# Performance work log

Hardware: AMD Instinct MI355X
Metric: run time of the kernel (lower is better)

## Reference

```python
import jax, jax.numpy as jnp
from jax import lax
import numpy as np

N = 32768; K = 8; M = 8192; G = 32; EF = 128

def _lrelu(x):
    return jnp.where(x > 0, x, 0.01 * x)

def _pc_res(x, W1, b1, W2, b2):
    h = _lrelu(x @ W1 + b1) @ W2 + b2
    return _lrelu(h + x)

def _conv3d(x, w, b):
    dn = ('NCDHW', 'OIDHW', 'NCDHW')
    return lax.conv_general_dilated(x, w, (1, 1, 1), 'SAME', dimension_numbers=dn) + b[None, :, None, None, None]

def setup_inputs():
    key = jax.random.key(0)
    ks = jax.random.split(key, 32)
    f32 = jnp.float32
    pc_KNN_idx = jax.random.randint(ks[0], (N * K,), 0, N, dtype=jnp.int32)
    pc_KNN_xyz = jax.random.normal(ks[1], (N * K, 3), dtype=f32)
    flat = jax.random.permutation(ks[2], G * G * G)[:M]  # unique voxel coords -> deterministic scatter
    voxel_xyz_int = jnp.stack([flat // (G * G), (flat // G) % G, flat % G], axis=1).astype(jnp.int32)
    voxel_KNN_idx = jax.random.randint(ks[3], (M * K,), 0, N, dtype=jnp.int32)
    voxel_KNN_xyz = jax.random.normal(ks[4], (M * K, 3), dtype=f32)
    s = 0.05
    def rn(i, shape):
        return jax.random.normal(ks[i], shape, dtype=f32) * s
    return dict(
        pc_KNN_idx=pc_KNN_idx, pc_KNN_xyz=pc_KNN_xyz, voxel_xyz_int=voxel_xyz_int,
        voxel_KNN_idx=voxel_KNN_idx, voxel_KNN_xyz=voxel_KNN_xyz,
        pcf_W1=rn(5, (3, EF)), pcf_b1=rn(6, (EF,)), pcf_W2=rn(7, (EF, EF)), pcf_b2=rn(8, (EF,)),
        pcres_W1=rn(9, (7, EF, EF)), pcres_b1=rn(10, (7, EF)),
        pcres_W2=rn(11, (7, EF, EF)), pcres_b2=rn(12, (7, EF)),
        pcc_W1=rn(13, (6, EF + 3, EF)), pcc_b1=rn(14, (6, EF)),
        pcc_W2=rn(15, (6, EF, EF)), pcc_b2=rn(16, (6, EF)),
        r3_Wc1=rn(17, (8, EF, EF, 3, 3, 3)), r3_bc1=rn(18, (8, EF)),
        r3_Wc2=rn(19, (8, EF, EF, 1, 1, 1)), r3_bc2=rn(20, (8, EF)),
        lin1_W=rn(21, (EF, EF)), lin1_b=rn(22, (EF,)),
        lin2_W=rn(23, (EF, EF)), lin2_b=rn(24, (EF,)),
        linb_W=rn(25, (EF, 3)), linb_b=rn(26, (3,)),
    )

def reference(pc_KNN_idx, pc_KNN_xyz, voxel_xyz_int, voxel_KNN_idx, voxel_KNN_xyz,
              pcf_W1, pcf_b1, pcf_W2, pcf_b2,
              pcres_W1, pcres_b1, pcres_W2, pcres_b2,
              pcc_W1, pcc_b1, pcc_W2, pcc_b2,
              r3_Wc1, r3_bc1, r3_Wc2, r3_bc2,
              lin1_W, lin1_b, lin2_W, lin2_b, linb_W, linb_b):
    # pc_conv_first: MLP on KNN relative xyz, max-pool over K neighbors -> [N, EF]
    out = _lrelu(pc_KNN_xyz @ pcf_W1 + pcf_b1) @ pcf_W2 + pcf_b2
    out = jnp.max(out.reshape(-1, K, EF), axis=1)
    out = _lrelu(out)
    out = _pc_res(out, pcres_W1[0], pcres_b1[0], pcres_W2[0], pcres_b2[0])
    for i in range(6):
        idx = pc_KNN_idx if i < 5 else voxel_KNN_idx
        xyz = pc_KNN_xyz if i < 5 else voxel_KNN_xyz
        g = jnp.concatenate([out[idx], xyz], axis=1)            # [R*K, EF+3]
        h = _lrelu(g @ pcc_W1[i] + pcc_b1[i]) @ pcc_W2[i] + pcc_b2[i]
        out = _lrelu(jnp.max(h.reshape(-1, K, EF), axis=1))     # [R, EF]
        out = _pc_res(out, pcres_W1[i + 1], pcres_b1[i + 1], pcres_W2[i + 1], pcres_b2[i + 1])
    # scatter voxel features into a dense grid (coords are unique)
    vi = voxel_xyz_int - jnp.min(voxel_xyz_int, axis=0)
    grid = jnp.zeros((G, G, G, EF), jnp.float32).at[vi[:, 0], vi[:, 1], vi[:, 2]].set(out)
    x = grid.transpose(3, 0, 1, 2)[None]                        # [1, EF, G, G, G]
    for i in range(8):
        y = _lrelu(_conv3d(x, r3_Wc1[i], r3_bc1[i]))
        y = _conv3d(y, r3_Wc2[i], r3_bc2[i])
        x = _lrelu(y + x)
    out = x[0].transpose(1, 2, 3, 0)[vi[:, 0], vi[:, 1], vi[:, 2]]  # gather back [M, EF]
    out = _lrelu(out @ lin1_W + lin1_b)
    out = _lrelu(out @ lin2_W + lin2_b)
    return jax.nn.sigmoid(out @ linb_W + linb_b)                # out_bool head [M, 3]
```

## Files before the change

### kernel.cpp

```cpp
#include <hip/hip_runtime.h>
#include <math.h>

#define EF 128
#define NPTS 32768
#define KNN 8
#define MVOX 8192
#define GDIM 32
#define NVOXG (GDIM*GDIM*GDIM)

typedef __attribute__((ext_vector_type(8))) short bfrag;
typedef __attribute__((ext_vector_type(4))) float f32x4;

__device__ __forceinline__ float lrelu(float x) { return x > 0.f ? x : 0.01f * x; }
__device__ __forceinline__ short f2b(float f) {
    unsigned u = __float_as_uint(f);
    return (short)((u + 0x7fff + ((u >> 16) & 1)) >> 16);
}
#define MFMA(a,b,c) __builtin_amdgcn_mfma_f32_16x16x32_bf16((a),(b),(c),0,0,0)
__device__ __forceinline__ int swz(int row, int bytecol) {
    return row * 256 + (bytecol ^ ((row & 7) << 4));
}

__global__ void k_pack_w(const float* __restrict__ src, short* __restrict__ dst,
                         int K_real, int n_steps, int k_str, int c_str) {
    int t = blockIdx.x * 256 + threadIdx.x;
    int total = n_steps * 4096;
    if (t >= total) return;
    int r = t & 7, l = (t >> 3) & 63, ct = (t >> 9) & 7, s = t >> 12;
    int k = s * 32 + (l >> 4) * 8 + r;
    int col = ct * 16 + (l & 15);
    float v = (k < K_real) ? src[(size_t)k * k_str + (size_t)col * c_str] : 0.f;
    dst[t] = f2b(v);
}
__global__ void k_pack_wc1(const float* __restrict__ src, short* __restrict__ dst) {
    int t = blockIdx.x * 256 + threadIdx.x;
    if (t >= 108 * 4096) return;
    int r = t & 7, l = (t >> 3) & 63, ct = (t >> 9) & 7, s = t >> 12;
    int tap = s >> 2;
    int ci = (s & 3) * 32 + (l >> 4) * 8 + r;
    int col = ct * 16 + (l & 15);
    dst[t] = f2b(src[((size_t)col * 128 + ci) * 27 + tap]);
}


__global__ __launch_bounds__(512) void k_pcfirst(
    const float* __restrict__ xyz, const short* __restrict__ w1p, const float* __restrict__ b1,
    const short* __restrict__ w2p, const float* __restrict__ b2,
    const short* __restrict__ rw1p, const float* __restrict__ rb1,
    const short* __restrict__ rw2p, const float* __restrict__ rb2,
    float* __restrict__ out32, short* __restrict__ out16) {
    __shared__ __align__(16) char tb[32768];
    int wid = threadIdx.x >> 6, lane = threadIdx.x & 63, lrow = lane & 15, lq = lane >> 4;
    int wm = wid >> 2, wn = wid & 3;
    int rowbase = blockIdx.x * 128;
    f32x4 zv = {0.f, 0.f, 0.f, 0.f};
    {
        f32x4 acc1[4][2];
        #pragma unroll
        for (int rt = 0; rt < 4; ++rt) { acc1[rt][0] = zv; acc1[rt][1] = zv; }
        bfrag Bv[2];
        #pragma unroll
        for (int ct = 0; ct < 2; ++ct) Bv[ct] = ((const bfrag*)w1p)[(wn * 2 + ct) * 64 + lane];
        #pragma unroll
        for (int rt = 0; rt < 4; ++rt) {
            bfrag a4;
            #pragma unroll
            for (int r = 0; r < 8; ++r) a4[r] = 0;
            if (lq == 0) {
                int gr = rowbase + wm * 64 + rt * 16 + lrow;
                a4[0] = f2b(xyz[gr * 3]); a4[1] = f2b(xyz[gr * 3 + 1]); a4[2] = f2b(xyz[gr * 3 + 2]);
            }
            #pragma unroll
            for (int ct = 0; ct < 2; ++ct) acc1[rt][ct] = MFMA(a4, Bv[ct], acc1[rt][ct]);
        }
        float bb1[2];
        #pragma unroll
        for (int ct = 0; ct < 2; ++ct) bb1[ct] = b1[wn * 32 + ct * 16 + lrow];
        #pragma unroll
        for (int rt = 0; rt < 4; ++rt)
            #pragma unroll
            for (int ct = 0; ct < 2; ++ct)
                #pragma unroll
                for (int r = 0; r < 4; ++r) {
                    int row = wm * 64 + rt * 16 + lq * 4 + r, col = wn * 32 + ct * 16 + lrow;
                    *(short*)(tb + swz(row, col * 2)) = f2b(lrelu(acc1[rt][ct][r] + bb1[ct]));
                }
    }
    __syncthreads();
    float bb2[2];
    #pragma unroll
    for (int ct = 0; ct < 2; ++ct) bb2[ct] = b2[wn * 32 + ct * 16 + lrow];
    f32x4 acc[4][2];
    #pragma unroll
    for (int rt = 0; rt < 4; ++rt) { acc[rt][0] = zv; acc[rt][1] = zv; }
    const bfrag* bp2 = (const bfrag*)w2p;
    #pragma unroll
    for (int s = 0; s < 4; ++s) {
        bfrag Bv[2];
        #pragma unroll
        for (int ct = 0; ct < 2; ++ct) Bv[ct] = bp2[(s * 8 + wn * 2 + ct) * 64 + lane];
        bfrag av[4];
        #pragma unroll
        for (int rt = 0; rt < 4; ++rt) {
            int row = wm * 64 + rt * 16 + lrow;
            av[rt] = *(const bfrag*)(tb + swz(row, s * 64 + lq * 16));
        }
        #pragma unroll
        for (int ct = 0; ct < 2; ++ct)
            #pragma unroll
            for (int rt = 0; rt < 4; ++rt) acc[rt][ct] = MFMA(av[rt], Bv[ct], acc[rt][ct]);
    }
    float pv[4][2];
    #pragma unroll
    for (int rt = 0; rt < 4; ++rt)
        #pragma unroll
        for (int ct = 0; ct < 2; ++ct) {
            float m = -INFINITY;
            #pragma unroll
            for (int r = 0; r < 4; ++r) m = fmaxf(m, acc[rt][ct][r] + bb2[ct]);
            m = fmaxf(m, __shfl_xor(m, 16, 64));
            pv[rt][ct] = lrelu(m);
        }
    __syncthreads();
    float* xf = (float*)(tb + 4096);
    char*  tres = tb + 12544;
    if ((lq & 1) == 0) {
        #pragma unroll
        for (int rt = 0; rt < 4; ++rt)
            #pragma unroll
            for (int ct = 0; ct < 2; ++ct) {
                int row = wm * 8 + rt * 2 + (lq >> 1), col = wn * 32 + ct * 16 + lrow;
                *(short*)(tb + swz(row, col * 2)) = f2b(pv[rt][ct]);
                xf[row * 130 + col] = pv[rt][ct];
            }
    }
    __syncthreads();
    {
        f32x4 r1 = zv;
        #pragma unroll
        for (int s = 0; s < 4; ++s) {
            bfrag B = ((const bfrag*)rw1p)[(s * 8 + wid) * 64 + lane];
            bfrag a = *(const bfrag*)(tb + swz(lrow, s * 64 + lq * 16));
            r1 = MFMA(a, B, r1);
        }
        float rb1v = rb1[wid * 16 + lrow];
        #pragma unroll
        for (int r = 0; r < 4; ++r) {
            int row = lq * 4 + r;
            *(short*)(tres + swz(row, (wid * 16 + lrow) * 2)) = f2b(lrelu(r1[r] + rb1v));
        }
    }
    __syncthreads();
    {
        f32x4 r2 = zv;
        #pragma unroll
        for (int s = 0; s < 4; ++s) {
            bfrag B = ((const bfrag*)rw2p)[(s * 8 + wid) * 64 + lane];
            bfrag a = *(const bfrag*)(tres + swz(lrow, s * 64 + lq * 16));
            r2 = MFMA(a, B, r2);
        }
        float rb2v = rb2[wid * 16 + lrow];
        int p0 = blockIdx.x * 16;
        #pragma unroll
        for (int r = 0; r < 4; ++r) {
            int row = lq * 4 + r, col = wid * 16 + lrow;
            float v = lrelu(r2[r] + rb2v + xf[row * 130 + col]);
            size_t o = (size_t)(p0 + row) * 128 + col;
            out16[o] = f2b(v);
            if (out32) out32[o] = v;
        }
    }
}

__global__ __launch_bounds__(512) void k_pcconv(
    const short* __restrict__ fin16, const int* __restrict__ idx, const float* __restrict__ xyz,
    const short* __restrict__ w1p, const float* __restrict__ b1,
    const short* __restrict__ w2p, const float* __restrict__ b2,
    const short* __restrict__ rw1p, const float* __restrict__ rb1,
    const short* __restrict__ rw2p, const float* __restrict__ rb2,
    float* __restrict__ out32, short* __restrict__ out16) {
    __shared__ __align__(16) char tb[32768];
    int wid = threadIdx.x >> 6, lane = threadIdx.x & 63, lrow = lane & 15, lq = lane >> 4;
    int wm = wid >> 2, wn = wid & 3;
    int rowbase = blockIdx.x * 128;
    f32x4 zv = {0.f, 0.f, 0.f, 0.f};
    {
        int srow = threadIdx.x >> 2, sseg = threadIdx.x & 3;
        int nb = idx[rowbase + srow];
        const bfrag* src = (const bfrag*)(fin16 + (size_t)nb * 128);
        #pragma unroll
        for (int j = 0; j < 4; ++j) {
            int seg = sseg + j * 4;
            bfrag v = src[seg];
            *(bfrag*)(tb + swz(srow, seg * 16)) = v;
        }
    }
    __syncthreads();
    float bb1[2], bb2[2];
    #pragma unroll
    for (int ct = 0; ct < 2; ++ct) {
        bb1[ct] = b1[wn * 32 + ct * 16 + lrow];
        bb2[ct] = b2[wn * 32 + ct * 16 + lrow];
    }
    f32x4 acc[4][2];
    #pragma unroll
    for (int rt = 0; rt < 4; ++rt) { acc[rt][0] = zv; acc[rt][1] = zv; }
    const bfrag* bp1 = (const bfrag*)w1p;
    #pragma unroll
    for (int s = 0; s < 4; ++s) {
        bfrag Bv[2];
        #pragma unroll
        for (int ct = 0; ct < 2; ++ct) Bv[ct] = bp1[(s * 8 + wn * 2 + ct) * 64 + lane];
        bfrag av[4];
        #pragma unroll
        for (int rt = 0; rt < 4; ++rt) {
            int row = wm * 64 + rt * 16 + lrow;
            av[rt] = *(const bfrag*)(tb + swz(row, s * 64 + lq * 16));
        }
        #pragma unroll
        for (int ct = 0; ct < 2; ++ct)
            #pragma unroll
            for (int rt = 0; rt < 4; ++rt) acc[rt][ct] = MFMA(av[rt], Bv[ct], acc[rt][ct]);
    }
    {
        bfrag Bv[2];
        #pragma unroll
        for (int ct = 0; ct < 2; ++ct) Bv[ct] = bp1[(32 + wn * 2 + ct) * 64 + lane];
        #pragma unroll
        for (int rt = 0; rt < 4; ++rt) {
            bfrag a4;
            #pragma unroll
            for (int r = 0; r < 8; ++r) a4[r] = 0;
            if (lq == 0) {
                int gr = rowbase + wm * 64 + rt * 16 + lrow;
                a4[0] = f2b(xyz[gr * 3]); a4[1] = f2b(xyz[gr * 3 + 1]); a4[2] = f2b(xyz[gr * 3 + 2]);
            }
            #pragma unroll
            for (int ct = 0; ct < 2; ++ct) acc[rt][ct] = MFMA(a4, Bv[ct], acc[rt][ct]);
        }
    }
    __syncthreads();
    #pragma unroll
    for (int rt = 0; rt < 4; ++rt)
        #pragma unroll
        for (int ct = 0; ct < 2; ++ct)
            #pragma unroll
            for (int r = 0; r < 4; ++r) {
                int row = wm * 64 + rt * 16 + lq * 4 + r, col = wn * 32 + ct * 16 + lrow;
                *(short*)(tb + swz(row, col * 2)) = f2b(lrelu(acc[rt][ct][r] + bb1[ct]));
            }
    __syncthreads();
    f32x4 acc2[4][2];
    #pragma unroll
    for (int rt = 0; rt < 4; ++rt) { acc2[rt][0] = zv; acc2[rt][1] = zv; }
    const bfrag* bp2 = (const bfrag*)w2p;
    #pragma unroll
    for (int s = 0; s < 4; ++s) {
        bfrag Bv[2];
        #pragma unroll
        for (int ct = 0; ct < 2; ++ct) Bv[ct] = bp2[(s * 8 + wn * 2 + ct) * 64 + lane];
        bfrag av[4];
        #pragma unroll
        for (int rt = 0; rt < 4; ++rt) {
            int row = wm * 64 + rt * 16 + lrow;
            av[rt] = *(const bfrag*)(tb + swz(row, s * 64 + lq * 16));
        }
        #pragma unroll
        for (int ct = 0; ct < 2; ++ct)
            #pragma unroll
            for (int rt = 0; rt < 4; ++rt) acc2[rt][ct] = MFMA(av[rt], Bv[ct], acc2[rt][ct]);
    }
    float pv[4][2];
    #pragma unroll
    for (int rt = 0; rt < 4; ++rt)
        #pragma unroll
        for (int ct = 0; ct < 2; ++ct) {
            float m = -INFINITY;
            #pragma unroll
            for (int r = 0; r < 4; ++r) m = fmaxf(m, acc2[rt][ct][r] + bb2[ct]);
            m = fmaxf(m, __shfl_xor(m, 16, 64));
            pv[rt][ct] = lrelu(m);
        }
    __syncthreads();
    float* xf = (float*)(tb + 4096);
    char*  tres = tb + 12544;
    if ((lq & 1) == 0) {
        #pragma unroll
        for (int rt = 0; rt < 4; ++rt)
            #pragma unroll
            for (int ct = 0; ct < 2; ++ct) {
                int row = wm * 8 + rt * 2 + (lq >> 1), col = wn * 32 + ct * 16 + lrow;
                *(short*)(tb + swz(row, col * 2)) = f2b(pv[rt][ct]);
                xf[row * 130 + col] = pv[rt][ct];
            }
    }
    __syncthreads();
    {
        f32x4 r1 = zv;
        #pragma unroll
        for (int s = 0; s < 4; ++s) {
            bfrag B = ((const bfrag*)rw1p)[(s * 8 + wid) * 64 + lane];
            bfrag a = *(const bfrag*)(tb + swz(lrow, s * 64 + lq * 16));
            r1 = MFMA(a, B, r1);
        }
        float rb1v = rb1[wid * 16 + lrow];
        #pragma unroll
        for (int r = 0; r < 4; ++r) {
            int row = lq * 4 + r;
            *(short*)(tres + swz(row, (wid * 16 + lrow) * 2)) = f2b(lrelu(r1[r] + rb1v));
        }
    }
    __syncthreads();
    {
        f32x4 r2 = zv;
        #pragma unroll
        for (int s = 0; s < 4; ++s) {
            bfrag B = ((const bfrag*)rw2p)[(s * 8 + wid) * 64 + lane];
            bfrag a = *(const bfrag*)(tres + swz(lrow, s * 64 + lq * 16));
            r2 = MFMA(a, B, r2);
        }
        float rb2v = rb2[wid * 16 + lrow];
        int p0 = blockIdx.x * 16;
        #pragma unroll
        for (int r = 0; r < 4; ++r) {
            int row = lq * 4 + r, col = wid * 16 + lrow;
            float v = lrelu(r2[r] + rb2v + xf[row * 130 + col]);
            size_t o = (size_t)(p0 + row) * 128 + col;
            out16[o] = f2b(v);
            if (out32) out32[o] = v;
        }
    }
}

__global__ __launch_bounds__(512) void k_conv3(
    const float* __restrict__ gin32, const short* __restrict__ gin16,
    const short* __restrict__ w1p, const float* __restrict__ b1,
    const short* __restrict__ w2p, const float* __restrict__ b2,
    float* __restrict__ gout32, short* __restrict__ gout16) {
    __shared__ __align__(16) char Ab[65536];
    int wid = threadIdx.x >> 6, lane = threadIdx.x & 63, lrow = lane & 15, lq = lane >> 4;
    int kg = wid & 1, wn = (wid >> 1) & 1, wm = wid >> 2;
    int va = blockIdx.x >> 3, vb0 = (blockIdx.x & 7) * 4;
    bfrag zf;
    #pragma unroll
    for (int r = 0; r < 8; ++r) zf[r] = 0;
    f32x4 zv = {0.f, 0.f, 0.f, 0.f};
    f32x4 acc[4][4];
    #pragma unroll
    for (int rt = 0; rt < 4; ++rt)
        #pragma unroll
        for (int ct = 0; ct < 4; ++ct) acc[rt][ct] = zv;
    const bfrag* bp1 = (const bfrag*)w1p;

    #pragma unroll 1
    for (int dai = 0; dai < 3; ++dai) {
        __syncthreads();
        {
            int aa = va + dai - 1;
            bool aok = (unsigned)aa < 32u;
            #pragma unroll
            for (int j = 0; j < 6; ++j) {
                int task = (int)threadIdx.x + j * 512;
                int srow = task >> 4, seg = task & 15;
                int bl = srow >> 5, c = srow & 31;
                int sb = vb0 - 1 + bl;
                bool ok = aok && ((unsigned)sb < 32u);
                size_t gb = ok ? ((size_t)((aa * 32 + sb) * 32 + c) * 128 + seg * 8) : 0;
                bfrag v = *((const bfrag*)gin16 + gb / 8);
                *(bfrag*)(Ab + swz(srow, seg * 16)) = ok ? v : zf;
            }
        }
        __syncthreads();
        #pragma unroll
        for (int t9 = 0; t9 < 9; ++t9) {
            int db = t9 / 3 - 1, dc = t9 % 3 - 1;
            int tap = dai * 9 + t9;
            #pragma unroll
            for (int ss = 0; ss < 2; ++ss) {
                int s = kg * 2 + ss;
                bfrag Bv[4];
                #pragma unroll
                for (int ct = 0; ct < 4; ++ct)
                    Bv[ct] = bp1[((tap * 4 + s) * 8 + wn * 4 + ct) * 64 + lane];
                bfrag av[4];
                #pragma unroll
                for (int rt = 0; rt < 4; ++rt) {
                    int ci = ((rt & 1) << 4) + lrow + dc;
                    bool ok = (unsigned)ci < 32u;
                    int srow2 = (wm * 2 + db + 1 + (rt >> 1)) * 32 + (ok ? ci : 0);
                    bfrag t = *(const bfrag*)(Ab + swz(srow2, s * 64 + lq * 16));
                    av[rt] = ok ? t : zf;
                }
                #pragma unroll
                for (int ct = 0; ct < 4; ++ct)
                    #pragma unroll
                    for (int rt = 0; rt < 4; ++rt) acc[rt][ct] = MFMA(av[rt], Bv[ct], acc[rt][ct]);
            }
        }
    }
    __syncthreads();
    if (kg == 1) {
        int p = wm * 2 + wn;
        #pragma unroll
        for (int rt = 0; rt < 4; ++rt)
            #pragma unroll
            for (int ct = 0; ct < 4; ++ct)
                *(f32x4*)(Ab + p * 16384 + ((rt * 4 + ct) * 64 + lane) * 16) = acc[rt][ct];
    }
    __syncthreads();
    if (kg == 0) {
        int p = wm * 2 + wn;
        #pragma unroll
        for (int rt = 0; rt < 4; ++rt)
            #pragma unroll
            for (int ct = 0; ct < 4; ++ct)
                acc[rt][ct] += *(const f32x4*)(Ab + p * 16384 + ((rt * 4 + ct) * 64 + lane) * 16);
    }
    __syncthreads();
    if (kg == 0) {
        float bb1[4];
        #pragma unroll
        for (int ct = 0; ct < 4; ++ct) bb1[ct] = b1[wn * 64 + ct * 16 + lrow];
        #pragma unroll
        for (int rt = 0; rt < 4; ++rt)
            #pragma unroll
            for (int ct = 0; ct < 4; ++ct)
                #pragma unroll
                for (int r = 0; r < 4; ++r) {
                    int row = wm * 64 + rt * 16 + lq * 4 + r, col = wn * 64 + ct * 16 + lrow;
                    *(short*)(Ab + swz(row, col * 2)) = f2b(lrelu(acc[rt][ct][r] + bb1[ct]));
                }
    }
    __syncthreads();
    int wm2 = wid >> 2, wn2 = wid & 3;
    float bb2[2];
    #pragma unroll
    for (int ct = 0; ct < 2; ++ct) bb2[ct] = b2[wn2 * 32 + ct * 16 + lrow];
    f32x4 acc2[4][2];
    #pragma unroll
    for (int rt = 0; rt < 4; ++rt) { acc2[rt][0] = zv; acc2[rt][1] = zv; }
    const bfrag* bp2 = (const bfrag*)w2p;
    #pragma unroll
    for (int s = 0; s < 4; ++s) {
        bfrag Bv[2];
        #pragma unroll
        for (int ct = 0; ct < 2; ++ct) Bv[ct] = bp2[(s * 8 + wn2 * 2 + ct) * 64 + lane];
        bfrag av[4];
        #pragma unroll
        for (int rt = 0; rt < 4; ++rt) {
            int row = wm2 * 64 + rt * 16 + lrow;
            av[rt] = *(const bfrag*)(Ab + swz(row, s * 64 + lq * 16));
        }
        #pragma unroll
        for (int ct = 0; ct < 2; ++ct)
            #pragma unroll
            for (int rt = 0; rt < 4; ++rt) acc2[rt][ct] = MFMA(av[rt], Bv[ct], acc2[rt][ct]);
    }
    #pragma unroll
    for (int rt = 0; rt < 4; ++rt)
        #pragma unroll
        for (int ct = 0; ct < 2; ++ct)
            #pragma unroll
            for (int r = 0; r < 4; ++r) {
                int row = wm2 * 64 + rt * 16 + lq * 4 + r;
                int voxel = (va * 32 + vb0 + (row >> 5)) * 32 + (row & 31);
                size_t o = (size_t)voxel * 128 + wn2 * 32 + ct * 16 + lrow;
                float v = lrelu(acc2[rt][ct][r] + bb2[ct] + gin32[o]);
                gout32[o] = v; gout16[o] = f2b(v);
            }
}

__global__ __launch_bounds__(512) void k_head(
    const short* __restrict__ g16, const int* __restrict__ vx, const int* __restrict__ vmin,
    const short* __restrict__ w1p, const float* __restrict__ b1,
    const short* __restrict__ w2p, const float* __restrict__ b2,
    const float* __restrict__ W3, const float* __restrict__ b3,
    float* __restrict__ out) {
    __shared__ __align__(16) char tb[16384];
    __shared__ float t2[64][129];
    int wid = threadIdx.x >> 6, lane = threadIdx.x & 63, lrow = lane & 15, lq = lane >> 4;
    int rowbase = blockIdx.x * 64;
    int goff[4];
    #pragma unroll
    for (int rt = 0; rt < 4; ++rt) {
        int m = rowbase + rt * 16 + lrow;
        int v0 = vx[m * 3 + 0] - vmin[0];
        int v1 = vx[m * 3 + 1] - vmin[1];
        int v2 = vx[m * 3 + 2] - vmin[2];
        goff[rt] = ((v0 * 32 + v1) * 32 + v2) * 128;
    }
    float bb1 = b1[wid * 16 + lrow], bb2 = b2[wid * 16 + lrow];
    f32x4 zv = {0.f, 0.f, 0.f, 0.f};
    f32x4 acc[4];
    #pragma unroll
    for (int rt = 0; rt < 4; ++rt) acc[rt] = zv;
    const bfrag* bp1 = (const bfrag*)w1p;
    #pragma unroll
    for (int s = 0; s < 4; ++s) {
        bfrag B = bp1[(s * 8 + wid) * 64 + lane];
        #pragma unroll
        for (int rt = 0; rt < 4; ++rt) {
            bfrag a = *((const bfrag*)(g16 + goff[rt]) + s * 4 + lq);
            acc[rt] = MFMA(a, B, acc[rt]);
        }
    }
    #pragma unroll
    for (int rt = 0; rt < 4; ++rt)
        #pragma unroll
        for (int r = 0; r < 4; ++r) {
            int row = rt * 16 + lq * 4 + r, col = wid * 16 + lrow;
            *(short*)(tb + swz(row, col * 2)) = f2b(lrelu(acc[rt][r] + bb1));
        }
    __syncthreads();
    f32x4 acc2[4];
    #pragma unroll
    for (int rt = 0; rt < 4; ++rt) acc2[rt] = zv;
    const bfrag* bp2 = (const bfrag*)w2p;
    #pragma unroll
    for (int s = 0; s < 4; ++s) {
        bfrag B = bp2[(s * 8 + wid) * 64 + lane];
        #pragma unroll
        for (int rt = 0; rt < 4; ++rt) {
            int row = rt * 16 + lrow;
            bfrag av = *(const bfrag*)(tb + swz(row, s * 64 + lq * 16));
            acc2[rt] = MFMA(av, B, acc2[rt]);
        }
    }
    #pragma unroll
    for (int rt = 0; rt < 4; ++rt)
        #pragma unroll
        for (int r = 0; r < 4; ++r) {
            int row = rt * 16 + lq * 4 + r, col = wid * 16 + lrow;
            t2[row][col] = lrelu(acc2[rt][r] + bb2);
        }
    __syncthreads();
    if (threadIdx.x < 192) {
        int row = threadIdx.x & 63, c = threadIdx.x >> 6;
        float s = b3[c];
        #pragma unroll 4
        for (int k = 0; k < 128; ++k) s += t2[row][k] * W3[k * 3 + c];
        out[(size_t)(rowbase + row) * 3 + c] = 1.f / (1.f + expf(-s));
    }
}

__global__ void k_vmin(const int* __restrict__ vx, int M, int* __restrict__ vmin) {
    __shared__ int sm[3 * 256];
    int t = threadIdx.x;
    int m0 = 0x7fffffff, m1 = 0x7fffffff, m2 = 0x7fffffff;
    for (int i = t; i < M; i += 256) {
        m0 = min(m0, vx[i * 3 + 0]); m1 = min(m1, vx[i * 3 + 1]); m2 = min(m2, vx[i * 3 + 2]);
    }
    sm[t] = m0; sm[256 + t] = m1; sm[512 + t] = m2;
    __syncthreads();
    for (int s = 128; s > 0; s >>= 1) {
        if (t < s) {
            sm[t] = min(sm[t], sm[t + s]);
            sm[256 + t] = min(sm[256 + t], sm[256 + t + s]);
            sm[512 + t] = min(sm[512 + t], sm[512 + t + s]);
        }
        __syncthreads();
    }
    if (t == 0) { vmin[0] = sm[0]; vmin[1] = sm[256]; vmin[2] = sm[512]; }
}

__global__ void k_scatter(const float* __restrict__ vf, const int* __restrict__ vx,
                          const int* __restrict__ vmin, float* __restrict__ g32, short* __restrict__ g16) {
    int m = blockIdx.x, j = threadIdx.x;
    int v0 = vx[m * 3 + 0] - vmin[0];
    int v1 = vx[m * 3 + 1] - vmin[1];
    int v2 = vx[m * 3 + 2] - vmin[2];
    size_t o = (size_t)(((v0 * GDIM) + v1) * GDIM + v2) * EF + j;
    float v = vf[(size_t)m * EF + j];
    g32[o] = v; g16[o] = f2b(v);
}

extern "C" void kernel_launch(void* const* d_in, const int* in_sizes, int n_in,
                              void* d_out, int out_size, void* d_ws, size_t ws_size,
                              hipStream_t stream) {
    const int*   pc_idx  = (const int*)  d_in[0];
    const float* pc_xyz  = (const float*)d_in[1];
    const int*   vox_int = (const int*)  d_in[2];
    const int*   vox_idx = (const int*)  d_in[3];
    const float* vox_xyz = (const float*)d_in[4];
    const float* pcf_W1  = (const float*)d_in[5];
    const float* pcf_b1  = (const float*)d_in[6];
    const float* pcf_W2  = (const float*)d_in[7];
    const float* pcf_b2  = (const float*)d_in[8];
    const float* pcres_W1 = (const float*)d_in[9];
    const float* pcres_b1 = (const float*)d_in[10];
    const float* pcres_W2 = (const float*)d_in[11];
    const float* pcres_b2 = (const float*)d_in[12];
    const float* pcc_W1  = (const float*)d_in[13];
    const float* pcc_b1  = (const float*)d_in[14];
    const float* pcc_W2  = (const float*)d_in[15];
    const float* pcc_b2  = (const float*)d_in[16];
    const float* r3_Wc1  = (const float*)d_in[17];
    const float* r3_bc1  = (const float*)d_in[18];
    const float* r3_Wc2  = (const float*)d_in[19];
    const float* r3_bc2  = (const float*)d_in[20];
    const float* lin1_W  = (const float*)d_in[21];
    const float* lin1_b  = (const float*)d_in[22];
    const float* lin2_W  = (const float*)d_in[23];
    const float* lin2_b  = (const float*)d_in[24];
    const float* linb_W  = (const float*)d_in[25];
    const float* linb_b  = (const float*)d_in[26];

    const size_t NE = (size_t)NPTS * EF;
    float* A32 = (float*)d_ws;
    float* B32 = A32 + NE;
    short* A16 = (short*)(B32 + NE);
    short* B16 = A16 + NE;
    float* Y32 = (float*)(B16 + NE);
    short* Y16 = (short*)(Y32 + NE);
    short* pcf_w1p = Y16 + NE;
    short* pcf_w2p = pcf_w1p + 1 * 4096;
    short* pcc_w1p = pcf_w2p + 4 * 4096;
    short* pcc_w2p = pcc_w1p + 6 * 5 * 4096;
    short* pcr_w1p = pcc_w2p + 6 * 4 * 4096;
    short* pcr_w2p = pcr_w1p + 7 * 4 * 4096;
    short* wc2p    = pcr_w2p + 7 * 4 * 4096;
    short* lin1p   = wc2p    + 8 * 4 * 4096;
    short* lin2p   = lin1p   + 4 * 4096;
    short* wc1p    = lin2p   + 4 * 4096;
    int*   vmin    = (int*)(wc1p + 108 * 4096);

    k_pack_w<<<16, 256, 0, stream>>>(pcf_W1, pcf_w1p, 3, 1, 128, 1);
    k_pack_w<<<64, 256, 0, stream>>>(pcf_W2, pcf_w2p, 128, 4, 128, 1);
    for (int i = 0; i < 6; ++i) {
        k_pack_w<<<80, 256, 0, stream>>>(pcc_W1 + (size_t)i * 131 * 128, pcc_w1p + (size_t)i * 5 * 4096, 131, 5, 128, 1);
        k_pack_w<<<64, 256, 0, stream>>>(pcc_W2 + (size_t)i * 128 * 128, pcc_w2p + (size_t)i * 4 * 4096, 128, 4, 128, 1);
    }
    for (int i = 0; i < 7; ++i) {
        k_pack_w<<<64, 256, 0, stream>>>(pcres_W1 + (size_t)i * 128 * 128, pcr_w1p + (size_t)i * 4 * 4096, 128, 4, 128, 1);
        k_pack_w<<<64, 256, 0, stream>>>(pcres_W2 + (size_t)i * 128 * 128, pcr_w2p + (size_t)i * 4 * 4096, 128, 4, 128, 1);
    }
    for (int i = 0; i < 8; ++i)
        k_pack_w<<<64, 256, 0, stream>>>(r3_Wc2 + (size_t)i * 128 * 128, wc2p + (size_t)i * 4 * 4096, 128, 4, 1, 128);
    k_pack_w<<<64, 256, 0, stream>>>(lin1_W, lin1p, 128, 4, 128, 1);
    k_pack_w<<<64, 256, 0, stream>>>(lin2_W, lin2p, 128, 4, 128, 1);

    k_pcfirst<<<NPTS * KNN / 128, 512, 0, stream>>>(pc_xyz, pcf_w1p, pcf_b1, pcf_w2p, pcf_b2,
        pcr_w1p, pcres_b1, pcr_w2p, pcres_b2, nullptr, A16);
    short* cur16 = A16; short* nxt16 = B16;
    for (int i = 0; i < 5; ++i) {
        k_pcconv<<<NPTS * KNN / 128, 512, 0, stream>>>(cur16, pc_idx, pc_xyz,
            pcc_w1p + (size_t)i * 5 * 4096, pcc_b1 + i * EF,
            pcc_w2p + (size_t)i * 4 * 4096, pcc_b2 + i * EF,
            pcr_w1p + (size_t)(i + 1) * 4 * 4096, pcres_b1 + (i + 1) * EF,
            pcr_w2p + (size_t)(i + 1) * 4 * 4096, pcres_b2 + (i + 1) * EF,
            nullptr, nxt16);
        short* t = cur16; cur16 = nxt16; nxt16 = t;
    }
    k_pcconv<<<MVOX * KNN / 128, 512, 0, stream>>>(cur16, vox_idx, vox_xyz,
        pcc_w1p + (size_t)5 * 5 * 4096, pcc_b1 + 5 * EF,
        pcc_w2p + (size_t)5 * 4 * 4096, pcc_b2 + 5 * EF,
        pcr_w1p + (size_t)6 * 4 * 4096, pcres_b1 + 6 * EF,
        pcr_w2p + (size_t)6 * 4 * 4096, pcres_b2 + 6 * EF,
        A32, A16);

    k_vmin<<<1, 256, 0, stream>>>(vox_int, MVOX, vmin);
    hipMemsetAsync(B32, 0, NE * sizeof(float), stream);
    hipMemsetAsync(B16, 0, NE * sizeof(short), stream);
    k_scatter<<<MVOX, 128, 0, stream>>>(A32, vox_int, vmin, B32, B16);

    float* cur32 = B32; short* curg = B16;
    float* nxt32 = Y32; short* nxtg = Y16;
    for (int i = 0; i < 8; ++i) {
        k_pack_wc1<<<1728, 256, 0, stream>>>(r3_Wc1 + (size_t)i * 128 * 128 * 27, wc1p);
        k_conv3<<<256, 512, 0, stream>>>(cur32, curg, wc1p, r3_bc1 + i * EF,
                                         wc2p + (size_t)i * 4 * 4096, r3_bc2 + i * EF,
                                         nxt32, nxtg);
        float* t32 = cur32; cur32 = nxt32; nxt32 = t32;
        short* t16 = curg; curg = nxtg; nxtg = t16;
    }

    k_head<<<MVOX / 64, 512, 0, stream>>>(curg, vox_int, vmin,
                                          lin1p, lin1_b, lin2p, lin2_b, linb_W, linb_b,
                                          (float*)d_out);
}
```

Before: 714.4 us.

## Double-buffer conv3 input slabs and prefetch weight fragments across taps

```diff
diff --git a/kernel.cpp b/kernel.cpp
--- a/kernel.cpp
+++ b/kernel.cpp
@@ -337,10 +337,13 @@
     const short* __restrict__ w1p, const float* __restrict__ b1,
     const short* __restrict__ w2p, const float* __restrict__ b2,
     float* __restrict__ gout32, short* __restrict__ gout16) {
-    __shared__ __align__(16) char Ab[65536];
+    __shared__ __align__(16) char Ab[98304];
     int wid = threadIdx.x >> 6, lane = threadIdx.x & 63, lrow = lane & 15, lq = lane >> 4;
     int kg = wid & 1, wn = (wid >> 1) & 1, wm = wid >> 2;
-    int va = blockIdx.x >> 3, vb0 = (blockIdx.x & 7) * 4;
+    int bid = (int)blockIdx.x;
+    bid = (bid & 7) * 32 + (bid >> 3);
+    int va = bid >> 3, vb0 = (bid & 7) * 4;
+    int stid = threadIdx.x;
     bfrag zf;
     #pragma unroll
     for (int r = 0; r < 8; ++r) zf[r] = 0;
@@ -352,53 +355,89 @@
         for (int ct = 0; ct < 4; ++ct) acc[rt][ct] = zv;
     const bfrag* bp1 = (const bfrag*)w1p;
 
+    bfrag Bc[4], Bn[4];
+    #pragma unroll
+    for (int ct = 0; ct < 4; ++ct) Bc[ct] = bp1[((kg * 2) * 8 + wn * 4 + ct) * 64 + lane];
+
+    {
+        int aa = va - 1;
+        bool aok = (unsigned)aa < 32u;
+        #pragma unroll
+        for (int j = 0; j < 6; ++j) {
+            int task = stid + j * 512;
+            int srow = task >> 4, seg = task & 15;
+            int bl = srow >> 5, c = srow & 31;
+            int sb = vb0 - 1 + bl;
+            bool ok = aok && ((unsigned)sb < 32u);
+            size_t gb = ok ? ((size_t)((aa * 32 + sb) * 32 + c) * 16 + seg) : 0;
+            bfrag v = ((const bfrag*)gin16)[gb];
+            *(bfrag*)(Ab + swz(srow, seg * 16)) = ok ? v : zf;
+        }
+    }
+    __syncthreads();
+
     #pragma unroll 1
     for (int dai = 0; dai < 3; ++dai) {
-        __syncthreads();
-        {
-            int aa = va + dai - 1;
+        bfrag st[6]; bool oks[6];
+        if (dai < 2) {
+            int aa = va + dai;
             bool aok = (unsigned)aa < 32u;
             #pragma unroll
             for (int j = 0; j < 6; ++j) {
-                int task = (int)threadIdx.x + j * 512;
+                int task = stid + j * 512;
                 int srow = task >> 4, seg = task & 15;
                 int bl = srow >> 5, c = srow & 31;
                 int sb = vb0 - 1 + bl;
-                bool ok = aok && ((unsigned)sb < 32u);
-                size_t gb = ok ? ((size_t)((aa * 32 + sb) * 32 + c) * 128 + seg * 8) : 0;
-                bfrag v = *((const bfrag*)gin16 + gb / 8);
-                *(bfrag*)(Ab + swz(srow, seg * 16)) = ok ? v : zf;
-            }
-        }
-        __syncthreads();
-        #pragma unroll
-        for (int t9 = 0; t9 < 9; ++t9) {
-            int db = t9 / 3 - 1, dc = t9 % 3 - 1;
-            int tap = dai * 9 + t9;
-            #pragma unroll
-            for (int ss = 0; ss < 2; ++ss) {
-                int s = kg * 2 + ss;
-                bfrag Bv[4];
+                oks[j] = aok && ((unsigned)sb < 32u);
+                size_t gb = oks[j] ? ((size_t)((aa * 32 + sb) * 32 + c) * 16 + seg) : 0;
+                st[j] = ((const bfrag*)gin16)[gb];
+            }
+        }
+        const char* slab = Ab + (dai & 1) * 49152;
+        __builtin_amdgcn_s_setprio(1);
+        #pragma unroll
+        for (int g = 0; g < 18; ++g) {
+            int gg = dai * 18 + g;
+            if (gg + 1 < 54) {
+                int ggn = gg + 1;
+                int tapn = (ggn / 18) * 9 + ((ggn % 18) >> 1);
+                int sn = kg * 2 + (ggn & 1);
                 #pragma unroll
                 for (int ct = 0; ct < 4; ++ct)
-                    Bv[ct] = bp1[((tap * 4 + s) * 8 + wn * 4 + ct) * 64 + lane];
-                bfrag av[4];
+                    Bn[ct] = bp1[((tapn * 4 + sn) * 8 + wn * 4 + ct) * 64 + lane];
+            }
+            int t9 = g >> 1, ss = g & 1;
+            int db = t9 / 3 - 1, dc = t9 % 3 - 1;
+            int s = kg * 2 + ss;
+            bfrag av[4];
+            #pragma unroll
+            for (int rt = 0; rt < 4; ++rt) {
+                int ci = ((rt & 1) << 4) + lrow + dc;
+                bool ok = (unsigned)ci < 32u;
+                int srow2 = (wm * 2 + db + 1 + (rt >> 1)) * 32 + (ok ? ci : 0);
+                bfrag t = *(const bfrag*)(slab + swz(srow2, s * 64 + lq * 16));
+                av[rt] = ok ? t : zf;
+            }
+            #pragma unroll
+            for (int ct = 0; ct < 4; ++ct)
                 #pragma unroll
-                for (int rt = 0; rt < 4; ++rt) {
-                    int ci = ((rt & 1) << 4) + lrow + dc;
-                    bool ok = (unsigned)ci < 32u;
-                    int srow2 = (wm * 2 + db + 1 + (rt >> 1)) * 32 + (ok ? ci : 0);
-                    bfrag t = *(const bfrag*)(Ab + swz(srow2, s * 64 + lq * 16));
-                    av[rt] = ok ? t : zf;
-                }
-                #pragma unroll
-                for (int ct = 0; ct < 4; ++ct)
-                    #pragma unroll
-                    for (int rt = 0; rt < 4; ++rt) acc[rt][ct] = MFMA(av[rt], Bv[ct], acc[rt][ct]);
-            }
-        }
-    }
-    __syncthreads();
+                for (int rt = 0; rt < 4; ++rt) acc[rt][ct] = MFMA(av[rt], Bc[ct], acc[rt][ct]);
+            #pragma unroll
+            for (int ct = 0; ct < 4; ++ct) Bc[ct] = Bn[ct];
+        }
+        __builtin_amdgcn_s_setprio(0);
+        if (dai < 2) {
+            char* nb = Ab + ((dai + 1) & 1) * 49152;
+            #pragma unroll
+            for (int j = 0; j < 6; ++j) {
+                int task = stid + j * 512;
+                int srow = task >> 4, seg = task & 15;
+                *(bfrag*)(nb + swz(srow, seg * 16)) = oks[j] ? st[j] : zf;
+            }
+        }
+        __syncthreads();
+    }
+
     if (kg == 1) {
         int p = wm * 2 + wn;
         #pragma unroll
@@ -410,26 +449,20 @@
     __syncthreads();
     if (kg == 0) {
         int p = wm * 2 + wn;
+        float bb1[4];
+        #pragma unroll
+        for (int ct = 0; ct < 4; ++ct) bb1[ct] = b1[wn * 64 + ct * 16 + lrow];
         #pragma unroll
         for (int rt = 0; rt < 4; ++rt)
             #pragma unroll
-            for (int ct = 0; ct < 4; ++ct)
-                acc[rt][ct] += *(const f32x4*)(Ab + p * 16384 + ((rt * 4 + ct) * 64 + lane) * 16);
-    }
-    __syncthreads();
-    if (kg == 0) {
-        float bb1[4];
-        #pragma unroll
-        for (int ct = 0; ct < 4; ++ct) bb1[ct] = b1[wn * 64 + ct * 16 + lrow];
-        #pragma unroll
-        for (int rt = 0; rt < 4; ++rt)
-            #pragma unroll
-            for (int ct = 0; ct < 4; ++ct)
+            for (int ct = 0; ct < 4; ++ct) {
+                f32x4 o = acc[rt][ct] + *(const f32x4*)(Ab + p * 16384 + ((rt * 4 + ct) * 64 + lane) * 16);
                 #pragma unroll
                 for (int r = 0; r < 4; ++r) {
                     int row = wm * 64 + rt * 16 + lq * 4 + r, col = wn * 64 + ct * 16 + lrow;
-                    *(short*)(Ab + swz(row, col * 2)) = f2b(lrelu(acc[rt][ct][r] + bb1[ct]));
+                    *(short*)(Ab + 65536 + swz(row, col * 2)) = f2b(lrelu(o[r] + bb1[ct]));
                 }
+            }
     }
     __syncthreads();
     int wm2 = wid >> 2, wn2 = wid & 3;
@@ -449,7 +482,7 @@
         #pragma unroll
         for (int rt = 0; rt < 4; ++rt) {
             int row = wm2 * 64 + rt * 16 + lrow;
-            av[rt] = *(const bfrag*)(Ab + swz(row, s * 64 + lq * 16));
+            av[rt] = *(const bfrag*)(Ab + 65536 + swz(row, s * 64 + lq * 16));
         }
         #pragma unroll
         for (int ct = 0; ct < 2; ++ct)
```

Result: slower. 874.5 us (+22.4%).
